# Performance work log

Hardware: AMD Instinct MI355X
Metric: run time of the kernel (lower is better)

## Reference

```python
import jax, jax.numpy as jnp
import numpy as np

N = 50000      # nodes
E = 640000     # edges
D = 128        # input/hidden dim
L = 3          # GIN layers
G = 256        # graphs in batch
LAT = 64       # latent dim
BN_EPS = 1e-5
SLOPE = 0.2    # LeakyReLU negative slope


def _leaky(h):
    return jnp.where(h >= 0, h, SLOPE * h)


def setup_inputs() -> dict:
    key = jax.random.key(0)
    ks = jax.random.split(key, 8)
    x = jax.random.normal(ks[0], (N, D), dtype=jnp.float32)
    edge_index = jax.random.randint(ks[1], (2, E), 0, N, dtype=jnp.int64)
    batch = jnp.sort(jax.random.randint(ks[2], (N,), 0, G, dtype=jnp.int64))
    W1 = jax.random.normal(ks[3], (L, D, D), dtype=jnp.float32) * 0.05
    W2 = jax.random.normal(ks[4], (L, D, D), dtype=jnp.float32) * 0.05
    fc_W = jax.random.normal(ks[5], (LAT, D), dtype=jnp.float32) * 0.05
    return {
        "x": x,
        "W1": W1,
        "b1": jnp.zeros((L, D), jnp.float32),
        "bn_g": jnp.ones((L, D), jnp.float32),
        "bn_b": jnp.zeros((L, D), jnp.float32),
        "bn_m": jnp.zeros((L, D), jnp.float32),
        "bn_v": jax.random.uniform(ks[6], (L, D), jnp.float32, 0.5, 1.5),
        "W2": W2,
        "b2": jnp.zeros((L, D), jnp.float32),
        "out_g": jnp.ones((D,), jnp.float32),
        "out_b": jnp.zeros((D,), jnp.float32),
        "out_m": jnp.zeros((D,), jnp.float32),
        "out_v": jax.random.uniform(ks[7], (D,), jnp.float32, 0.5, 1.5),
        "fc_W": fc_W,
        "fc_b": jnp.zeros((LAT,), jnp.float32),
        "edge_index": edge_index,
        "batch": batch,
    }


def reference(x, W1, b1, bn_g, bn_b, bn_m, bn_v, W2, b2,
              out_g, out_b, out_m, out_v, fc_W, fc_b,
              edge_index, batch):
    src, dst = edge_index[0], edge_index[1]
    for i in range(L):
        # GINConv: (1+eps)*x + sum_{j in N(i)} x_j  (eps=0 default)
        agg = x + jax.ops.segment_sum(x[src], dst, num_segments=N)
        # MLP: Linear -> LeakyReLU -> BatchNorm(eval) -> Linear -> LeakyReLU
        h = _leaky(agg @ W1[i].T + b1[i])
        h = (h - bn_m[i]) * jax.lax.rsqrt(bn_v[i] + BN_EPS) * bn_g[i] + bn_b[i]
        x = _leaky(h @ W2[i].T + b2[i])
        # dropout is identity in eval mode
    pooled = jax.ops.segment_sum(x, batch, num_segments=G)  # [G, D]
    out = (pooled - out_m) * jax.lax.rsqrt(out_v + BN_EPS) * out_g + out_b
    return out @ fc_W.T + fc_b  # [G, LAT]
```

## Files before the change

kernel.cpp:

```cpp
#include <hip/hip_runtime.h>
#include <cstdint>
#include <cstddef>

#define NN 50000
#define EE 640000
#define DD 128
#define LL 3
#define GG 256
#define LATD 64

typedef __attribute__((ext_vector_type(8))) __bf16 bf16x8;
typedef __attribute__((ext_vector_type(4))) float f32x4;

__device__ __forceinline__ unsigned short f2bf(float f) {
  __bf16 h = (__bf16)f;
  return __builtin_bit_cast(unsigned short, h);
}
__device__ __forceinline__ float bf2f(unsigned int u16) {
  unsigned int x = u16 << 16;
  return __builtin_bit_cast(float, x);
}
__device__ __forceinline__ void unpack8(uint4 v, float* f) {
  f[0] = bf2f(v.x & 0xffffu); f[1] = bf2f(v.x >> 16);
  f[2] = bf2f(v.y & 0xffffu); f[3] = bf2f(v.y >> 16);
  f[4] = bf2f(v.z & 0xffffu); f[5] = bf2f(v.z >> 16);
  f[6] = bf2f(v.w & 0xffffu); f[7] = bf2f(v.w >> 16);
}
__device__ __forceinline__ void acc8(uint4 v, float* f) {
  f[0] += bf2f(v.x & 0xffffu); f[1] += bf2f(v.x >> 16);
  f[2] += bf2f(v.y & 0xffffu); f[3] += bf2f(v.y >> 16);
  f[4] += bf2f(v.z & 0xffffu); f[5] += bf2f(v.z >> 16);
  f[6] += bf2f(v.w & 0xffffu); f[7] += bf2f(v.w >> 16);
}
__device__ __forceinline__ uint4 pack8(const float* f) {
  uint4 v;
  v.x = f2bf(f[0]) | ((unsigned)f2bf(f[1]) << 16);
  v.y = f2bf(f[2]) | ((unsigned)f2bf(f[3]) << 16);
  v.z = f2bf(f[4]) | ((unsigned)f2bf(f[5]) << 16);
  v.w = f2bf(f[6]) | ((unsigned)f2bf(f[7]) << 16);
  return v;
}

#define SWZ(byte_, row_) ((byte_) ^ (((row_) & 7) << 4))

__global__ __launch_bounds__(256) void cvt_kernel(const float4* __restrict__ x,
                                                  uint4* __restrict__ xb) {
  int t = blockIdx.x * 256 + threadIdx.x;
  float4 a = x[t * 2], b = x[t * 2 + 1];
  float f[8] = {a.x, a.y, a.z, a.w, b.x, b.y, b.z, b.w};
  xb[t] = pack8(f);
}

__global__ __launch_bounds__(256) void wcvt_kernel(const float* __restrict__ W1,
                                                   const float* __restrict__ W2,
                                                   uint4* __restrict__ wb) {
  int t = blockIdx.x * 256 + threadIdx.x;
  int m = t >> 11;
  int q = t & 2047;
  int byte = q * 16;
  int row = byte >> 8;
  int inner = byte & 255;
  int isrc = inner ^ ((row & 7) << 4);
  int k0 = isrc >> 1;
  const float* Wsrc = (m & 1) ? W2 : W1;
  const float* p = Wsrc + ((size_t)(m >> 1) * DD * DD + row * DD + k0);
  float4 f0 = ((const float4*)p)[0], f1 = ((const float4*)p)[1];
  float f[8] = {f0.x, f0.y, f0.z, f0.w, f1.x, f1.y, f1.z, f1.w};
  wb[(size_t)m * 2048 + q] = pack8(f);
}

__global__ __launch_bounds__(256) void hist_kernel(const int* __restrict__ dst,
                                                   int* __restrict__ counts, int E) {
  int e = blockIdx.x * blockDim.x + threadIdx.x;
  if (e < E) atomicAdd(&counts[dst[e]], 1);
}

__global__ __launch_bounds__(256) void scan1_kernel(const int* __restrict__ counts,
                                                    int* __restrict__ rp,
                                                    int* __restrict__ bsum, int n) {
  int i = blockIdx.x * 256 + threadIdx.x;
  int v = (i < n) ? counts[i] : 0;
  int lane = threadIdx.x & 63, w = threadIdx.x >> 6;
  int s = v;
#pragma unroll
  for (int off = 1; off < 64; off <<= 1) {
    int u = __shfl_up(s, off);
    if (lane >= off) s += u;
  }
  __shared__ int ws[4];
  if (lane == 63) ws[w] = s;
  __syncthreads();
  int add = 0;
#pragma unroll
  for (int k = 0; k < 4; ++k) if (k < w) add += ws[k];
  int incl = s + add;
  if (i < n) rp[i] = incl - v;
  if (threadIdx.x == 255) bsum[blockIdx.x] = incl;
}

__global__ __launch_bounds__(256) void scan2_kernel(int* __restrict__ bsum, int nb) {
  int t = threadIdx.x;
  int v = (t < nb) ? bsum[t] : 0;
  int lane = t & 63, w = t >> 6;
  int s = v;
#pragma unroll
  for (int off = 1; off < 64; off <<= 1) {
    int u = __shfl_up(s, off);
    if (lane >= off) s += u;
  }
  __shared__ int ws[4];
  if (lane == 63) ws[w] = s;
  __syncthreads();
  int add = 0;
#pragma unroll
  for (int k = 0; k < 4; ++k) if (k < w) add += ws[k];
  int incl = s + add;
  if (t < nb) bsum[t] = incl - v;
}

__global__ __launch_bounds__(256) void scan3_kernel(int* __restrict__ rp,
                                                    int* __restrict__ cursor,
                                                    const int* __restrict__ bsum, int n) {
  int i = blockIdx.x * 256 + threadIdx.x;
  if (i < n) {
    int v = rp[i] + bsum[blockIdx.x];
    rp[i] = v;
    cursor[i] = v;
  }
  if (i == 0) rp[n] = EE;
}

__global__ __launch_bounds__(256) void fill_kernel(const int* __restrict__ src,
                                                   const int* __restrict__ dst,
                                                   int* __restrict__ cursor,
                                                   int* __restrict__ col, int E) {
  int e = blockIdx.x * blockDim.x + threadIdx.x;
  if (e < E) {
    int p = atomicAdd(&cursor[dst[e]], 1);
    col[p] = src[e];
  }
}

__global__ __launch_bounds__(256, 4) void agg_kernel(const uint4* __restrict__ xin,
                                                     const int* __restrict__ row_ptr,
                                                     const int* __restrict__ colv,
                                                     uint4* __restrict__ agg, int n) {
  int tid = blockIdx.x * 256 + threadIdx.x;
  int node = tid >> 4;
  int c = tid & 15;
  if (node >= n) return;
  float acc[8];
  unpack8(xin[(size_t)node * 16 + c], acc);
  int s = row_ptr[node], e = row_ptr[node + 1];
  int j = s;
  for (; j + 8 <= e; j += 8) {
    int i0 = colv[j],     i1 = colv[j + 1], i2 = colv[j + 2], i3 = colv[j + 3];
    int i4 = colv[j + 4], i5 = colv[j + 5], i6 = colv[j + 6], i7 = colv[j + 7];
    uint4 v0 = xin[(size_t)i0 * 16 + c];
    uint4 v1 = xin[(size_t)i1 * 16 + c];
    uint4 v2 = xin[(size_t)i2 * 16 + c];
    uint4 v3 = xin[(size_t)i3 * 16 + c];
    uint4 v4 = xin[(size_t)i4 * 16 + c];
    uint4 v5 = xin[(size_t)i5 * 16 + c];
    uint4 v6 = xin[(size_t)i6 * 16 + c];
    uint4 v7 = xin[(size_t)i7 * 16 + c];
    acc8(v0, acc); acc8(v1, acc); acc8(v2, acc); acc8(v3, acc);
    acc8(v4, acc); acc8(v5, acc); acc8(v6, acc); acc8(v7, acc);
  }
  for (; j + 2 <= e; j += 2) {
    uint4 v0 = xin[(size_t)colv[j] * 16 + c];
    uint4 v1 = xin[(size_t)colv[j + 1] * 16 + c];
    acc8(v0, acc); acc8(v1, acc);
  }
  if (j < e) acc8(xin[(size_t)colv[j] * 16 + c], acc);
  agg[(size_t)node * 16 + c] = pack8(acc);
}

__global__ __launch_bounds__(512) void mlp128(
    const uint4* __restrict__ aggb, unsigned short* __restrict__ xout,
    const uint4* __restrict__ w1b, const uint4* __restrict__ w2b,
    const float* __restrict__ b1, const float* __restrict__ bng,
    const float* __restrict__ bnb, const float* __restrict__ bnm,
    const float* __restrict__ bnv, const float* __restrict__ b2, int n) {
  __shared__ __align__(16) char smem[98304];
  char* w1p = smem;
  char* w2p = smem + 32768;
  char* xp  = smem + 65536;

#pragma unroll
  for (int it = 0; it < 8; ++it) {
    int q = it * 512 + threadIdx.x;
    ((uint4*)w1p)[q] = w1b[q];
    ((uint4*)w2p)[q] = w2b[q];
  }

  int lane = threadIdx.x & 63;
  int c = lane & 15;
  int kq = lane >> 4;
  int wave = threadIdx.x >> 6;
  int r0 = wave * 16;

  float b1v[8], sv[8], tv[8], b2v[8];
#pragma unroll
  for (int ni = 0; ni < 8; ++ni) {
    int cc = ni * 16 + c;
    b1v[ni] = b1[cc];
    float s = bng[cc] * rsqrtf(bnv[cc] + 1e-5f);
    sv[ni] = s;
    tv[ni] = bnb[cc] - bnm[cc] * s;
    b2v[ni] = b2[cc];
  }

  for (int tile = blockIdx.x; tile * 128 < n; tile += 256) {
    int base = tile * 128;
#pragma unroll
    for (int it = 0; it < 4; ++it) {
      int t = it * 512 + threadIdx.x;
      int row = t >> 4, cc = t & 15;
      int grow = base + row;
      uint4 v = make_uint4(0, 0, 0, 0);
      if (grow < n) v = aggb[(size_t)grow * 16 + cc];
      *(uint4*)(xp + SWZ(row * 256 + cc * 16, row)) = v;
    }
    __syncthreads();

    f32x4 acc[8];
#pragma unroll
    for (int ni = 0; ni < 8; ++ni) acc[ni] = (f32x4){0.f, 0.f, 0.f, 0.f};

#pragma unroll
    for (int ks = 0; ks < 4; ++ks) {
      int row = r0 + c;
      bf16x8 a = *(const bf16x8*)(xp + SWZ(row * 256 + ks * 64 + kq * 16, row));
#pragma unroll
      for (int ni = 0; ni < 8; ++ni) {
        int wr = ni * 16 + c;
        bf16x8 bfr = *(const bf16x8*)(w1p + SWZ(wr * 256 + ks * 64 + kq * 16, wr));
        acc[ni] = __builtin_amdgcn_mfma_f32_16x16x32_bf16(a, bfr, acc[ni], 0, 0, 0);
      }
    }

#pragma unroll
    for (int ni = 0; ni < 8; ++ni)
#pragma unroll
      for (int r = 0; r < 4; ++r) {
        float h = acc[ni][r] + b1v[ni];
        h = h >= 0.f ? h : 0.2f * h;
        h = h * sv[ni] + tv[ni];
        int row = r0 + kq * 4 + r;
        *(__bf16*)(xp + SWZ(row * 256 + (ni * 16 + c) * 2, row)) = (__bf16)h;
      }
    __syncthreads();

#pragma unroll
    for (int ni = 0; ni < 8; ++ni) acc[ni] = (f32x4){0.f, 0.f, 0.f, 0.f};

#pragma unroll
    for (int ks = 0; ks < 4; ++ks) {
      int row = r0 + c;
      bf16x8 a = *(const bf16x8*)(xp + SWZ(row * 256 + ks * 64 + kq * 16, row));
#pragma unroll
      for (int ni = 0; ni < 8; ++ni) {
        int wr = ni * 16 + c;
        bf16x8 bfr = *(const bf16x8*)(w2p + SWZ(wr * 256 + ks * 64 + kq * 16, wr));
        acc[ni] = __builtin_amdgcn_mfma_f32_16x16x32_bf16(a, bfr, acc[ni], 0, 0, 0);
      }
    }

#pragma unroll
    for (int ni = 0; ni < 8; ++ni)
#pragma unroll
      for (int r = 0; r < 4; ++r) {
        float xo = acc[ni][r] + b2v[ni];
        xo = xo >= 0.f ? xo : 0.2f * xo;
        int grow = base + r0 + kq * 4 + r;
        if (grow < n) xout[(size_t)grow * DD + ni * 16 + c] = f2bf(xo);
      }
    __syncthreads();
  }
}

__global__ __launch_bounds__(256) void pool_kernel(const uint4* __restrict__ x,
                                                   const int* __restrict__ batch,
                                                   float* __restrict__ pooled, int n) {
  int gid = blockIdx.x * 256 + threadIdx.x;
  int grp = gid >> 4, c = gid & 15;
  int n0 = grp * 16;
  if (n0 >= n) return;
  float acc[8] = {0.f, 0.f, 0.f, 0.f, 0.f, 0.f, 0.f, 0.f};
  int curg = batch[n0];
  int end = n0 + 16 < n ? n0 + 16 : n;
  for (int node = n0; node < end; ++node) {
    int g = batch[node];
    if (g != curg) {
      float* p = pooled + (size_t)curg * DD + c * 8;
#pragma unroll
      for (int i = 0; i < 8; ++i) { atomicAdd(p + i, acc[i]); acc[i] = 0.f; }
      curg = g;
    }
    float tmp[8];
    unpack8(x[(size_t)node * 16 + c], tmp);
#pragma unroll
    for (int i = 0; i < 8; ++i) acc[i] += tmp[i];
  }
  float* p = pooled + (size_t)curg * DD + c * 8;
#pragma unroll
  for (int i = 0; i < 8; ++i) atomicAdd(p + i, acc[i]);
}

__global__ __launch_bounds__(128) void head_kernel(const float* __restrict__ pooled,
    const float* __restrict__ og, const float* __restrict__ ob,
    const float* __restrict__ om, const float* __restrict__ ov,
    const float* __restrict__ fcW, const float* __restrict__ fcb,
    float* __restrict__ out) {
  __shared__ float pb[DD];
  int g = blockIdx.x;
  int t = threadIdx.x;
  float s = og[t] * rsqrtf(ov[t] + 1e-5f);
  pb[t] = (pooled[(size_t)g * DD + t] - om[t]) * s + ob[t];
  __syncthreads();
  if (t < LATD) {
    float acc = fcb[t];
#pragma unroll 8
    for (int d = 0; d < DD; ++d) acc = fmaf(fcW[t * DD + d], pb[d], acc);
    out[(size_t)g * LATD + t] = acc;
  }
}

extern "C" void kernel_launch(void* const* d_in, const int* in_sizes, int n_in,
                              void* d_out, int out_size, void* d_ws, size_t ws_size,
                              hipStream_t stream) {
  const float* x   = (const float*)d_in[0];
  const float* W1  = (const float*)d_in[1];
  const float* b1  = (const float*)d_in[2];
  const float* bng = (const float*)d_in[3];
  const float* bnb = (const float*)d_in[4];
  const float* bnm = (const float*)d_in[5];
  const float* bnv = (const float*)d_in[6];
  const float* W2  = (const float*)d_in[7];
  const float* b2  = (const float*)d_in[8];
  const float* og  = (const float*)d_in[9];
  const float* ob  = (const float*)d_in[10];
  const float* om  = (const float*)d_in[11];
  const float* ov  = (const float*)d_in[12];
  const float* fcW = (const float*)d_in[13];
  const float* fcb = (const float*)d_in[14];
  const int* ei    = (const int*)d_in[15];
  const int* batch = (const int*)d_in[16];
  const int* src  = ei;
  const int* dstp = ei + EE;

  char* ws = (char*)d_ws;
  size_t off = 0;
  auto alloc = [&](size_t bytes) {
    void* p = ws + off;
    off += (bytes + 255) & ~(size_t)255;
    return p;
  };
  unsigned short* xb0  = (unsigned short*)alloc((size_t)NN * DD * 2);
  unsigned short* xb1  = (unsigned short*)alloc((size_t)NN * DD * 2);
  unsigned short* aggb = (unsigned short*)alloc((size_t)NN * DD * 2);
  uint4* wb     = (uint4*)alloc((size_t)6 * 2048 * 16);
  int* row_ptr  = (int*)alloc((NN + 1) * 4);
  int* cursor   = (int*)alloc(NN * 4);
  int* counts   = (int*)alloc(NN * 4);
  int* col      = (int*)alloc(EE * 4);
  int* bsum     = (int*)alloc(256 * 4);
  float* pooled = (float*)alloc(GG * DD * 4);

  hipMemsetAsync(counts, 0, NN * 4, stream);
  hipMemsetAsync(pooled, 0, GG * DD * 4, stream);

  cvt_kernel<<<3125, 256, 0, stream>>>((const float4*)x, (uint4*)xb0);
  wcvt_kernel<<<48, 256, 0, stream>>>(W1, W2, wb);

  const int NB = (NN + 255) / 256;
  hist_kernel<<<(EE + 255) / 256, 256, 0, stream>>>(dstp, counts, EE);
  scan1_kernel<<<NB, 256, 0, stream>>>(counts, row_ptr, bsum, NN);
  scan2_kernel<<<1, 256, 0, stream>>>(bsum, NB);
  scan3_kernel<<<NB, 256, 0, stream>>>(row_ptr, cursor, bsum, NN);
  fill_kernel<<<(EE + 255) / 256, 256, 0, stream>>>(src, dstp, cursor, col, EE);

  unsigned short* xcur = xb0;
  unsigned short* xnext = xb1;
  for (int i = 0; i < LL; ++i) {
    agg_kernel<<<(NN * 16 + 255) / 256, 256, 0, stream>>>(
        (const uint4*)xcur, row_ptr, col, (uint4*)aggb, NN);
    mlp128<<<256, 512, 0, stream>>>(
        (const uint4*)aggb, xnext,
        wb + (size_t)i * 4096, wb + (size_t)i * 4096 + 2048,
        b1 + i * DD, bng + i * DD, bnb + i * DD, bnm + i * DD, bnv + i * DD,
        b2 + i * DD, NN);
    unsigned short* t = xcur; xcur = xnext; xnext = t;
  }
  pool_kernel<<<(NN * 16 + 255) / 256, 256, 0, stream>>>(
      (const uint4*)xcur, batch, pooled, NN);
  head_kernel<<<GG, 128, 0, stream>>>(pooled, og, ob, om, ov, fcW, fcb, (float*)d_out);
}
```

Measured before the change: 240.6 us.

## Pad atomic counters to cache lines and split neighbor aggregation across two half-groups

Counts and cursor arrays are padded to one 64-byte line per node so the atomics in the histogram and fill kernels stop contending on shared cache lines. The aggregation kernel now assigns 32 threads per node: two halves each take alternating neighbors, then combine their partial sums with a cross-lane shuffle. This doubles thread-level parallelism and memory-level parallelism per node at the cost of more threads and a larger, sparser counter array plus a bigger memset. Occupancy hint is raised to 8 blocks.

Result: no change. 238.7 us (-0.8%).

```diff
diff --git a/kernel.cpp b/kernel.cpp
--- a/kernel.cpp
+++ b/kernel.cpp
@@ -42,6 +42,7 @@
 }
 
 #define SWZ(byte_, row_) ((byte_) ^ (((row_) & 7) << 4))
+#define CPAD 4
 
 __global__ __launch_bounds__(256) void cvt_kernel(const float4* __restrict__ x,
                                                   uint4* __restrict__ xb) {
@@ -72,14 +73,14 @@
 __global__ __launch_bounds__(256) void hist_kernel(const int* __restrict__ dst,
                                                    int* __restrict__ counts, int E) {
   int e = blockIdx.x * blockDim.x + threadIdx.x;
-  if (e < E) atomicAdd(&counts[dst[e]], 1);
+  if (e < E) atomicAdd(&counts[dst[e] << CPAD], 1);
 }
 
 __global__ __launch_bounds__(256) void scan1_kernel(const int* __restrict__ counts,
                                                     int* __restrict__ rp,
                                                     int* __restrict__ bsum, int n) {
   int i = blockIdx.x * 256 + threadIdx.x;
-  int v = (i < n) ? counts[i] : 0;
+  int v = (i < n) ? counts[i << CPAD] : 0;
   int lane = threadIdx.x & 63, w = threadIdx.x >> 6;
   int s = v;
 #pragma unroll
@@ -125,7 +126,7 @@
   if (i < n) {
     int v = rp[i] + bsum[blockIdx.x];
     rp[i] = v;
-    cursor[i] = v;
+    cursor[i << CPAD] = v;
   }
   if (i == 0) rp[n] = EE;
 }
@@ -136,44 +137,36 @@
                                                    int* __restrict__ col, int E) {
   int e = blockIdx.x * blockDim.x + threadIdx.x;
   if (e < E) {
-    int p = atomicAdd(&cursor[dst[e]], 1);
+    int p = atomicAdd(&cursor[dst[e] << CPAD], 1);
     col[p] = src[e];
   }
 }
 
-__global__ __launch_bounds__(256, 4) void agg_kernel(const uint4* __restrict__ xin,
+__global__ __launch_bounds__(256, 8) void agg_kernel(const uint4* __restrict__ xin,
                                                      const int* __restrict__ row_ptr,
                                                      const int* __restrict__ colv,
                                                      uint4* __restrict__ agg, int n) {
   int tid = blockIdx.x * 256 + threadIdx.x;
-  int node = tid >> 4;
+  int node = tid >> 5;
   int c = tid & 15;
+  int half = (tid >> 4) & 1;
   if (node >= n) return;
-  float acc[8];
-  unpack8(xin[(size_t)node * 16 + c], acc);
+  float acc[8] = {0.f, 0.f, 0.f, 0.f, 0.f, 0.f, 0.f, 0.f};
+  if (!half) unpack8(xin[(size_t)node * 16 + c], acc);
   int s = row_ptr[node], e = row_ptr[node + 1];
-  int j = s;
-  for (; j + 8 <= e; j += 8) {
-    int i0 = colv[j],     i1 = colv[j + 1], i2 = colv[j + 2], i3 = colv[j + 3];
-    int i4 = colv[j + 4], i5 = colv[j + 5], i6 = colv[j + 6], i7 = colv[j + 7];
+  int j = s + half;
+  for (; j + 6 < e; j += 8) {
+    int i0 = colv[j], i1 = colv[j + 2], i2 = colv[j + 4], i3 = colv[j + 6];
     uint4 v0 = xin[(size_t)i0 * 16 + c];
     uint4 v1 = xin[(size_t)i1 * 16 + c];
     uint4 v2 = xin[(size_t)i2 * 16 + c];
     uint4 v3 = xin[(size_t)i3 * 16 + c];
-    uint4 v4 = xin[(size_t)i4 * 16 + c];
-    uint4 v5 = xin[(size_t)i5 * 16 + c];
-    uint4 v6 = xin[(size_t)i6 * 16 + c];
-    uint4 v7 = xin[(size_t)i7 * 16 + c];
     acc8(v0, acc); acc8(v1, acc); acc8(v2, acc); acc8(v3, acc);
-    acc8(v4, acc); acc8(v5, acc); acc8(v6, acc); acc8(v7, acc);
-  }
-  for (; j + 2 <= e; j += 2) {
-    uint4 v0 = xin[(size_t)colv[j] * 16 + c];
-    uint4 v1 = xin[(size_t)colv[j + 1] * 16 + c];
-    acc8(v0, acc); acc8(v1, acc);
-  }
-  if (j < e) acc8(xin[(size_t)colv[j] * 16 + c], acc);
-  agg[(size_t)node * 16 + c] = pack8(acc);
+  }
+  for (; j < e; j += 2) acc8(xin[(size_t)colv[j] * 16 + c], acc);
+#pragma unroll
+  for (int i = 0; i < 8; ++i) acc[i] += __shfl_xor(acc[i], 16);
+  if (!half) agg[(size_t)node * 16 + c] = pack8(acc);
 }
 
 __global__ __launch_bounds__(512) void mlp128(
@@ -362,13 +355,13 @@
   unsigned short* aggb = (unsigned short*)alloc((size_t)NN * DD * 2);
   uint4* wb     = (uint4*)alloc((size_t)6 * 2048 * 16);
   int* row_ptr  = (int*)alloc((NN + 1) * 4);
-  int* cursor   = (int*)alloc(NN * 4);
-  int* counts   = (int*)alloc(NN * 4);
+  int* cursor   = (int*)alloc((size_t)NN * 64);
+  int* counts   = (int*)alloc((size_t)NN * 64);
   int* col      = (int*)alloc(EE * 4);
   int* bsum     = (int*)alloc(256 * 4);
   float* pooled = (float*)alloc(GG * DD * 4);
 
-  hipMemsetAsync(counts, 0, NN * 4, stream);
+  hipMemsetAsync(counts, 0, (size_t)NN * 64, stream);
   hipMemsetAsync(pooled, 0, GG * DD * 4, stream);
 
   cvt_kernel<<<3125, 256, 0, stream>>>((const float4*)x, (uint4*)xb0);
@@ -384,7 +377,7 @@
   unsigned short* xcur = xb0;
   unsigned short* xnext = xb1;
   for (int i = 0; i < LL; ++i) {
-    agg_kernel<<<(NN * 16 + 255) / 256, 256, 0, stream>>>(
+    agg_kernel<<<(NN * 32 + 255) / 256, 256, 0, stream>>>(
         (const uint4*)xcur, row_ptr, col, (uint4*)aggb, NN);
     mlp128<<<256, 512, 0, stream>>>(
         (const uint4*)aggb, xnext,
```

## Fuse prep kernels into one launch and pad atomic counters to 64 bytes

Applied to the files above, without the earlier changes.

Merges the x conversion, weight conversion and degree histogram kernels into a single launch that dispatches on block index, cutting two kernel launches. It also spreads the per-node counts and cursor arrays to one int per 64-byte slot so that atomics on neighbouring nodes hit separate cache lines. In exchange, the memset and the scan reads now touch sixteen times more memory (about 3.2 MB per array), and the scan's strided reads lose coalescing.

Result: faster. 232.0 us (-3.6%).

```diff
diff --git a/kernel.cpp b/kernel.cpp
--- a/kernel.cpp
+++ b/kernel.cpp
@@ -42,44 +42,47 @@
 }
 
 #define SWZ(byte_, row_) ((byte_) ^ (((row_) & 7) << 4))
-
-__global__ __launch_bounds__(256) void cvt_kernel(const float4* __restrict__ x,
-                                                  uint4* __restrict__ xb) {
-  int t = blockIdx.x * 256 + threadIdx.x;
-  float4 a = x[t * 2], b = x[t * 2 + 1];
-  float f[8] = {a.x, a.y, a.z, a.w, b.x, b.y, b.z, b.w};
-  xb[t] = pack8(f);
-}
-
-__global__ __launch_bounds__(256) void wcvt_kernel(const float* __restrict__ W1,
-                                                   const float* __restrict__ W2,
-                                                   uint4* __restrict__ wb) {
-  int t = blockIdx.x * 256 + threadIdx.x;
-  int m = t >> 11;
-  int q = t & 2047;
-  int byte = q * 16;
-  int row = byte >> 8;
-  int inner = byte & 255;
-  int isrc = inner ^ ((row & 7) << 4);
-  int k0 = isrc >> 1;
-  const float* Wsrc = (m & 1) ? W2 : W1;
-  const float* p = Wsrc + ((size_t)(m >> 1) * DD * DD + row * DD + k0);
-  float4 f0 = ((const float4*)p)[0], f1 = ((const float4*)p)[1];
-  float f[8] = {f0.x, f0.y, f0.z, f0.w, f1.x, f1.y, f1.z, f1.w};
-  wb[(size_t)m * 2048 + q] = pack8(f);
-}
-
-__global__ __launch_bounds__(256) void hist_kernel(const int* __restrict__ dst,
-                                                   int* __restrict__ counts, int E) {
-  int e = blockIdx.x * blockDim.x + threadIdx.x;
-  if (e < E) atomicAdd(&counts[dst[e]], 1);
+#define CPAD 4
+
+#define CVT_BLK 3125
+#define WCV_BLK 48
+#define HIST_BLK 2500
+__global__ __launch_bounds__(256) void prep_kernel(
+    const float4* __restrict__ x, uint4* __restrict__ xb,
+    const float* __restrict__ W1, const float* __restrict__ W2,
+    uint4* __restrict__ wb, const int* __restrict__ dst,
+    int* __restrict__ counts) {
+  int b = blockIdx.x;
+  if (b < CVT_BLK) {
+    int t = b * 256 + threadIdx.x;
+    float4 a = x[t * 2], bb = x[t * 2 + 1];
+    float f[8] = {a.x, a.y, a.z, a.w, bb.x, bb.y, bb.z, bb.w};
+    xb[t] = pack8(f);
+  } else if (b < CVT_BLK + WCV_BLK) {
+    int t = (b - CVT_BLK) * 256 + threadIdx.x;
+    int m = t >> 11;
+    int q = t & 2047;
+    int byte = q * 16;
+    int row = byte >> 8;
+    int inner = byte & 255;
+    int isrc = inner ^ ((row & 7) << 4);
+    int k0 = isrc >> 1;
+    const float* Wsrc = (m & 1) ? W2 : W1;
+    const float* p = Wsrc + ((size_t)(m >> 1) * DD * DD + row * DD + k0);
+    float4 f0 = ((const float4*)p)[0], f1 = ((const float4*)p)[1];
+    float f[8] = {f0.x, f0.y, f0.z, f0.w, f1.x, f1.y, f1.z, f1.w};
+    wb[(size_t)m * 2048 + q] = pack8(f);
+  } else {
+    int e = (b - CVT_BLK - WCV_BLK) * 256 + threadIdx.x;
+    atomicAdd(&counts[dst[e] << CPAD], 1);
+  }
 }
 
 __global__ __launch_bounds__(256) void scan1_kernel(const int* __restrict__ counts,
                                                     int* __restrict__ rp,
                                                     int* __restrict__ bsum, int n) {
   int i = blockIdx.x * 256 + threadIdx.x;
-  int v = (i < n) ? counts[i] : 0;
+  int v = (i < n) ? counts[i << CPAD] : 0;
   int lane = threadIdx.x & 63, w = threadIdx.x >> 6;
   int s = v;
 #pragma unroll
@@ -125,7 +128,7 @@
   if (i < n) {
     int v = rp[i] + bsum[blockIdx.x];
     rp[i] = v;
-    cursor[i] = v;
+    cursor[i << CPAD] = v;
   }
   if (i == 0) rp[n] = EE;
 }
@@ -136,7 +139,7 @@
                                                    int* __restrict__ col, int E) {
   int e = blockIdx.x * blockDim.x + threadIdx.x;
   if (e < E) {
-    int p = atomicAdd(&cursor[dst[e]], 1);
+    int p = atomicAdd(&cursor[dst[e] << CPAD], 1);
     col[p] = src[e];
   }
 }
@@ -362,20 +365,19 @@
   unsigned short* aggb = (unsigned short*)alloc((size_t)NN * DD * 2);
   uint4* wb     = (uint4*)alloc((size_t)6 * 2048 * 16);
   int* row_ptr  = (int*)alloc((NN + 1) * 4);
-  int* cursor   = (int*)alloc(NN * 4);
-  int* counts   = (int*)alloc(NN * 4);
+  int* cursor   = (int*)alloc((size_t)NN * 64);
+  int* counts   = (int*)alloc((size_t)NN * 64);
   int* col      = (int*)alloc(EE * 4);
   int* bsum     = (int*)alloc(256 * 4);
   float* pooled = (float*)alloc(GG * DD * 4);
 
-  hipMemsetAsync(counts, 0, NN * 4, stream);
+  hipMemsetAsync(counts, 0, (size_t)NN * 64, stream);
   hipMemsetAsync(pooled, 0, GG * DD * 4, stream);
 
-  cvt_kernel<<<3125, 256, 0, stream>>>((const float4*)x, (uint4*)xb0);
-  wcvt_kernel<<<48, 256, 0, stream>>>(W1, W2, wb);
+  prep_kernel<<<CVT_BLK + WCV_BLK + HIST_BLK, 256, 0, stream>>>(
+      (const float4*)x, (uint4*)xb0, W1, W2, wb, dstp, counts);
 
   const int NB = (NN + 255) / 256;
-  hist_kernel<<<(EE + 255) / 256, 256, 0, stream>>>(dstp, counts, EE);
   scan1_kernel<<<NB, 256, 0, stream>>>(counts, row_ptr, bsum, NN);
   scan2_kernel<<<1, 256, 0, stream>>>(bsum, NB);
   scan3_kernel<<<NB, 256, 0, stream>>>(row_ptr, cursor, bsum, NN);
```
